# Performance work log

Measured on AMD Instinct MI355X. Metric: run time of the kernel, lower is better.

The kernel has to match this reference:

```python
import jax, jax.numpy as jnp
import numpy as np


def setup_inputs() -> dict:
    key = jax.random.key(0)
    kx, ka, kw = jax.random.split(key, 3)
    B, H, N, F = 8, 4, 1024, 128
    NHID = 128
    x = jax.random.normal(kx, (B, H, N, F), dtype=jnp.float32)
    adj = jax.random.uniform(ka, (B, H, N, N), dtype=jnp.float32)
    W = jax.random.normal(kw, (F, NHID), dtype=jnp.float32) / np.float32(np.sqrt(F))
    b = jnp.zeros((NHID,), dtype=jnp.float32)
    return {"x": x, "adj": adj, "W": W, "b": b}


def reference(x, adj, W, b):
    # x: [B, H, N, F], adj: [B, H, N, N]
    B, H, N, F = x.shape
    G = B * H
    k = (N * N) // int(N ** 0.5)  # top-k entries kept per (b,h) matrix

    # --- sparse_adj: keep global top-k entries of each N*N matrix ---
    flat = adj.reshape(G, N * N)
    vals, idx = jax.lax.top_k(flat, k)                    # [G, k]
    sparse = jnp.zeros_like(flat).at[jnp.arange(G)[:, None], idx].set(vals)
    sparse = sparse.reshape(G, N, N)

    # --- norm: symmetrize, then D^{-1/2} A D^{-1/2} ---
    s = (sparse + jnp.swapaxes(sparse, 1, 2)) * 0.5
    deg = jnp.sum(s, axis=-1)                             # [G, N]
    dinv = jnp.where(deg > 0, deg ** -0.5, 0.0)           # inf -> 0 as in torch
    norm_adj = dinv[:, :, None] * s * dinv[:, None, :]    # [G, N, N]

    # --- GIN conv with edge weights (eps = 0): ((1+eps)x + A_norm x) W + b ---
    # edge-list message passing over nonzeros of norm_adj == dense matmul
    xf = x.reshape(G, N, F)
    agg = jnp.einsum('gij,gjf->gif', norm_adj, xf)
    h = jax.nn.gelu((xf + agg) @ W + b, approximate=False)

    out = h.reshape(B, H, N, -1)                          # dropout: eval mode (identity)
    adj_copy = norm_adj                                   # [(B H), N, N]
    return out, adj_copy
```

## Files before the change

### kernel.cpp

```cpp
#include <hip/hip_runtime.h>
#include <math.h>

#define GG 32
#define NN1 1024
#define FF 128
#define MAT (NN1*NN1)
#define KKEEP 32768
#define NBINS 4096
#define CAP 8192
#define LCAP 1024
#define TIECAP 64
#define BINLO 1311
#define BINHI 1760

typedef __attribute__((ext_vector_type(8))) short short8;
typedef __attribute__((ext_vector_type(4))) float floatx4;
typedef __attribute__((ext_vector_type(8))) unsigned short ushort8;

__device__ __forceinline__ int fbin(float v) {
    int b = (int)((v - 0.95f) * 81920.0f);
    b = b < 0 ? 0 : (b > NBINS - 1 ? NBINS - 1 : b);
    return b;
}
__device__ __forceinline__ unsigned short f2bf(float f) {
    union { float f; unsigned u; } x; x.f = f;
    unsigned r = x.u + 0x7fffu + ((x.u >> 16) & 1u);
    return (unsigned short)(r >> 16);
}
__device__ __forceinline__ float bf2f(unsigned short h) {
    union { unsigned u; float f; } x; x.u = ((unsigned)h) << 16;
    return x.f;
}
__device__ __forceinline__ float gelu(float v) {
    return 0.5f * v * (1.0f + erff(v * 0.70710678118654752f));
}

__global__ __launch_bounds__(256) void k_histgather(const float* __restrict__ adj,
                                                    unsigned* __restrict__ hist,
                                                    uint2* __restrict__ cand,
                                                    unsigned* __restrict__ candCount) {
    __shared__ unsigned lh[NBINS];
    __shared__ uint2 lcand[LCAP];
    __shared__ unsigned lcnt;
    __shared__ unsigned gbase;
    int g = blockIdx.x >> 4, seg = blockIdx.x & 15;
    for (int i = threadIdx.x; i < NBINS; i += 256) lh[i] = 0;
    if (threadIdx.x == 0) lcnt = 0;
    __syncthreads();
    const float4* p = (const float4*)(adj + (size_t)g * MAT + (size_t)seg * 65536);
    for (int i = threadIdx.x; i < 16384; i += 256) {
        float4 v = p[i];
        unsigned base = (unsigned)(seg * 65536 + i * 4);
        float vv[4] = {v.x, v.y, v.z, v.w};
#pragma unroll
        for (int d = 0; d < 4; ++d) {
            if (vv[d] >= 0.95f) {
                int b = fbin(vv[d]);
                atomicAdd(&lh[b], 1u);
                if (b >= BINLO && b <= BINHI) {
                    unsigned pos = atomicAdd(&lcnt, 1u);
                    if (pos < LCAP) {
                        lcand[pos].x = __float_as_uint(vv[d]);
                        lcand[pos].y = base + (unsigned)d;
                    }
                }
            }
        }
    }
    __syncthreads();
    unsigned* gh = hist + g * NBINS;
    for (int i = threadIdx.x; i < NBINS; i += 256)
        if (lh[i]) atomicAdd(&gh[i], lh[i]);
    unsigned n = lcnt; if (n > LCAP) n = LCAP;
    if (threadIdx.x == 0) gbase = atomicAdd(&candCount[g], n);
    __syncthreads();
    unsigned gb = gbase;
    uint2* cg = cand + (size_t)g * CAP;
    for (unsigned i = threadIdx.x; i < n; i += 256) {
        unsigned pos = gb + i;
        if (pos < CAP) cg[pos] = lcand[i];
    }
}

__global__ __launch_bounds__(256) void k_selbin(const unsigned* __restrict__ hist,
                                                unsigned* __restrict__ binSel,
                                                unsigned* __restrict__ needArr) {
    int g = blockIdx.x;
    __shared__ unsigned csum[256];
    __shared__ unsigned after[256];
    const unsigned* gh = hist + g * NBINS;
    int t = threadIdx.x;
    unsigned s = 0;
    for (int i = 0; i < 16; ++i) s += gh[t * 16 + i];
    csum[t] = s;
    __syncthreads();
    if (t == 0) {
        unsigned run = 0;
        for (int c = 255; c >= 0; --c) { after[c] = run; run += csum[c]; }
    }
    __syncthreads();
    if (after[t] < (unsigned)KKEEP && after[t] + csum[t] >= (unsigned)KKEEP) {
        unsigned cum = after[t];
        for (int b2 = t * 16 + 15; b2 >= t * 16; --b2) {
            unsigned h = gh[b2];
            cum += h;
            if (cum >= (unsigned)KKEEP) {
                binSel[g] = (unsigned)b2;
                needArr[g] = (unsigned)KKEEP - (cum - h);
                break;
            }
        }
    }
}

__global__ __launch_bounds__(256) void k_rank(const uint2* __restrict__ cand,
                                              const unsigned* __restrict__ candCount,
                                              const unsigned* __restrict__ binSel,
                                              const unsigned* __restrict__ needArr,
                                              float* __restrict__ thr,
                                              unsigned* __restrict__ tieIdx,
                                              unsigned* __restrict__ tieCount) {
    int g = blockIdx.x;
    __shared__ uint2 mem[256];
    __shared__ unsigned mb;
    __shared__ float sT;
    unsigned m = candCount[g]; if (m > CAP) m = CAP;
    unsigned bsel = binSel[g];
    unsigned need = needArr[g];
    const uint2* cg = cand + (size_t)g * CAP;
    int t = threadIdx.x;
    if (t == 0) mb = 0;
    __syncthreads();
    for (unsigned ci = t; ci < m; ci += 256) {
        float v = __uint_as_float(cg[ci].x);
        if ((unsigned)fbin(v) == bsel) {
            unsigned i = atomicAdd(&mb, 1u);
            if (i < 256) mem[i] = cg[ci];
        }
    }
    __syncthreads();
    unsigned M = mb; if (M > 256) M = 256;
    unsigned rk = 0; float v = 0.f; unsigned idx = 0;
    if (t < (int)M) {
        v = __uint_as_float(mem[t].x);
        idx = mem[t].y;
        for (unsigned j = 0; j < M; ++j) {
            float vj = __uint_as_float(mem[j].x);
            if (vj > v || (vj == v && mem[j].y < idx)) ++rk;
        }
        if (rk == need - 1) sT = v;
    }
    __syncthreads();
    float T = sT;
    if (t == 0) thr[g] = T;
    if (t < (int)M && v == T && rk < need) {
        unsigned pos = atomicAdd(&tieCount[g], 1u);
        if (pos < TIECAP) tieIdx[g * TIECAP + pos] = idx;
    }
}

__device__ __forceinline__ float keepf(float v, unsigned idx, float T,
                                       const unsigned* __restrict__ tie, unsigned tc) {
    if (v > T) return v;
    if (v == T) {
        for (unsigned i = 0; i < tc; ++i)
            if (tie[i] == idx) return v;
    }
    return 0.f;
}

__global__ __launch_bounds__(256) void k_sym(const float* __restrict__ adj,
                                             const float* __restrict__ thr,
                                             const unsigned* __restrict__ tieIdx,
                                             const unsigned* __restrict__ tieCount,
                                             float* __restrict__ sOut,
                                             float* __restrict__ deg) {
    __shared__ float Al[64 * 65];
    __shared__ float Bl[64 * 65];
    int g = blockIdx.x / 136;
    int pr = blockIdx.x % 136;
    int ti = 0, rem = pr;
    while (rem >= 16 - ti) { rem -= 16 - ti; ++ti; }
    int tj = ti + rem;
    int t = threadIdx.x;
    float T = thr[g];
    unsigned tc = tieCount[g];
    if (tc > TIECAP) tc = TIECAP;
    const unsigned* tie = tieIdx + g * TIECAP;
    const float* ag = adj + (size_t)g * MAT;
    float* sg = sOut + (size_t)g * MAT;
    float* dg = deg + g * NN1;
    int r0 = t >> 4;
    int c0 = (t & 15) << 2;
    int i0 = ti << 6, j0 = tj << 6;
    bool off = (ti != tj);
    float av[4][4], bv[4][4];
#pragma unroll
    for (int q = 0; q < 4; ++q) {
        int r = r0 + (q << 4);
        unsigned base = (unsigned)((i0 + r) * NN1 + j0 + c0);
        float4 v = *(const float4*)(ag + base);
        av[q][0] = keepf(v.x, base + 0, T, tie, tc);
        av[q][1] = keepf(v.y, base + 1, T, tie, tc);
        av[q][2] = keepf(v.z, base + 2, T, tie, tc);
        av[q][3] = keepf(v.w, base + 3, T, tie, tc);
        Al[r * 65 + c0 + 0] = av[q][0];
        Al[r * 65 + c0 + 1] = av[q][1];
        Al[r * 65 + c0 + 2] = av[q][2];
        Al[r * 65 + c0 + 3] = av[q][3];
    }
    if (off) {
#pragma unroll
        for (int q = 0; q < 4; ++q) {
            int r = r0 + (q << 4);
            unsigned base = (unsigned)((j0 + r) * NN1 + i0 + c0);
            float4 v = *(const float4*)(ag + base);
            bv[q][0] = keepf(v.x, base + 0, T, tie, tc);
            bv[q][1] = keepf(v.y, base + 1, T, tie, tc);
            bv[q][2] = keepf(v.z, base + 2, T, tie, tc);
            bv[q][3] = keepf(v.w, base + 3, T, tie, tc);
            Bl[r * 65 + c0 + 0] = bv[q][0];
            Bl[r * 65 + c0 + 1] = bv[q][1];
            Bl[r * 65 + c0 + 2] = bv[q][2];
            Bl[r * 65 + c0 + 3] = bv[q][3];
        }
    }
    __syncthreads();
#pragma unroll
    for (int q = 0; q < 4; ++q) {
        int r = r0 + (q << 4);
        const float* Tr = off ? Bl : Al;
        float s0 = 0.5f * (av[q][0] + Tr[(c0 + 0) * 65 + r]);
        float s1 = 0.5f * (av[q][1] + Tr[(c0 + 1) * 65 + r]);
        float s2 = 0.5f * (av[q][2] + Tr[(c0 + 2) * 65 + r]);
        float s3 = 0.5f * (av[q][3] + Tr[(c0 + 3) * 65 + r]);
        *(float4*)(sg + (size_t)(i0 + r) * NN1 + j0 + c0) = make_float4(s0, s1, s2, s3);
        float rs = s0 + s1 + s2 + s3;
        rs += __shfl_xor(rs, 1);
        rs += __shfl_xor(rs, 2);
        rs += __shfl_xor(rs, 4);
        rs += __shfl_xor(rs, 8);
        if ((t & 15) == 0) atomicAdd(&dg[i0 + r], rs);
    }
    if (off) {
#pragma unroll
        for (int q = 0; q < 4; ++q) {
            int r = r0 + (q << 4);
            float s0 = 0.5f * (bv[q][0] + Al[(c0 + 0) * 65 + r]);
            float s1 = 0.5f * (bv[q][1] + Al[(c0 + 1) * 65 + r]);
            float s2 = 0.5f * (bv[q][2] + Al[(c0 + 2) * 65 + r]);
            float s3 = 0.5f * (bv[q][3] + Al[(c0 + 3) * 65 + r]);
            *(float4*)(sg + (size_t)(j0 + r) * NN1 + i0 + c0) = make_float4(s0, s1, s2, s3);
            float rs = s0 + s1 + s2 + s3;
            rs += __shfl_xor(rs, 1);
            rs += __shfl_xor(rs, 2);
            rs += __shfl_xor(rs, 4);
            rs += __shfl_xor(rs, 8);
            if ((t & 15) == 0) atomicAdd(&dg[j0 + r], rs);
        }
    }
}

__global__ __launch_bounds__(256) void k_dinv(const float* __restrict__ deg,
                                              float* __restrict__ dinv) {
    int i = blockIdx.x * 256 + threadIdx.x;
    float d = deg[i];
    dinv[i] = (d > 0.f) ? (float)(1.0 / sqrt((double)d)) : 0.f;
}

__global__ __launch_bounds__(256) void k_y(const float* __restrict__ x,
                                           const float* __restrict__ W,
                                           unsigned short* __restrict__ Yh,
                                           unsigned short* __restrict__ Yl) {
    __shared__ float Xl[64 * 128];
    int bx = blockIdx.x;
    int g = bx & 31, chunk = bx >> 5;
    int r0 = chunk * 64;
    int t = threadIdx.x;
    const float* xg = x + ((size_t)g * NN1 + r0) * FF;
    for (int i = t; i < 2048; i += 256) ((float4*)Xl)[i] = ((const float4*)xg)[i];
    __syncthreads();
    int Rr = (t >> 5) * 8;
    int c4 = (t & 31) * 4;
    float acc[8][4];
#pragma unroll
    for (int i = 0; i < 8; ++i)
#pragma unroll
        for (int j = 0; j < 4; ++j) acc[i][j] = 0.f;
    for (int f = 0; f < 128; ++f) {
        float4 wv = *(const float4*)(W + (size_t)f * 128 + c4);
#pragma unroll
        for (int i = 0; i < 8; ++i) {
            float a = Xl[(Rr + i) * 128 + f];
            acc[i][0] += a * wv.x;
            acc[i][1] += a * wv.y;
            acc[i][2] += a * wv.z;
            acc[i][3] += a * wv.w;
        }
    }
#pragma unroll
    for (int cc = 0; cc < 4; ++cc) {
        int c = c4 + cc;
        size_t base = ((size_t)g * 128 + c) * NN1 + r0 + Rr;
        ushort8 hh, ll;
#pragma unroll
        for (int i = 0; i < 8; ++i) {
            float v = acc[i][cc];
            unsigned short h = f2bf(v);
            hh[i] = h;
            ll[i] = f2bf(v - bf2f(h));
        }
        *(ushort8*)(Yh + base) = hh;
        *(ushort8*)(Yl + base) = ll;
    }
}

__global__ __launch_bounds__(256) void k_ng1(const unsigned short* __restrict__ Yh,
                                             const unsigned short* __restrict__ Yl,
                                             const float* __restrict__ dinv,
                                             float* __restrict__ sadj,
                                             const float* __restrict__ bias,
                                             float* __restrict__ hout) {
    __shared__ unsigned short AhL[32 * 40];
    __shared__ unsigned short AlL[32 * 40];
    int bx = blockIdx.x;
    int g = bx & 31, panel = bx >> 5;
    int r0 = panel * 32;
    int t = threadIdx.x;
    int w = t >> 6, lane = t & 63;
    int q = lane >> 4, n16 = lane & 15;
    float* sg = sadj + (size_t)g * MAT;
    const float* dv = dinv + g * NN1;
    int srow = t >> 3, skc = (t & 7) << 2;
    float drow = dv[r0 + srow];
    int cbase = w * 32;
    const unsigned short* yhg = Yh + (size_t)g * 128 * NN1;
    const unsigned short* ylg = Yl + (size_t)g * 128 * NN1;
    const unsigned short* ybh[2], *ybl[2];
#pragma unroll
    for (int ct = 0; ct < 2; ++ct) {
        size_t co = (size_t)(cbase + 16 * ct + n16) * NN1;
        ybh[ct] = yhg + co;
        ybl[ct] = ylg + co;
    }
    floatx4 acc[2][2];
#pragma unroll
    for (int i = 0; i < 2; ++i)
#pragma unroll
        for (int j = 0; j < 2; ++j) acc[i][j] = (floatx4){0.f, 0.f, 0.f, 0.f};

    for (int kt = 0; kt < 32; ++kt) {
        int k0 = kt << 5;
        float4 dj = *(const float4*)(dv + k0 + skc);
        float* ap = sg + (size_t)(r0 + srow) * NN1 + k0 + skc;
        float4 v = *(const float4*)ap;
        v.x *= drow * dj.x; v.y *= drow * dj.y;
        v.z *= drow * dj.z; v.w *= drow * dj.w;
        *(float4*)ap = v;
        float vv[4] = {v.x, v.y, v.z, v.w};
        ushort4 hh, ll;
        unsigned short* hp = (unsigned short*)&hh;
        unsigned short* lp = (unsigned short*)&ll;
#pragma unroll
        for (int d = 0; d < 4; ++d) {
            unsigned short h = f2bf(vv[d]);
            hp[d] = h;
            lp[d] = f2bf(vv[d] - bf2f(h));
        }
        *(ushort4*)(&AhL[srow * 40 + skc]) = hh;
        *(ushort4*)(&AlL[srow * 40 + skc]) = ll;
        __syncthreads();
        short8 ah[2], al[2], bh[2], bl[2];
#pragma unroll
        for (int rt = 0; rt < 2; ++rt) {
            ah[rt] = *(const short8*)(&AhL[(16 * rt + n16) * 40 + q * 8]);
            al[rt] = *(const short8*)(&AlL[(16 * rt + n16) * 40 + q * 8]);
        }
#pragma unroll
        for (int ct = 0; ct < 2; ++ct) {
            bh[ct] = *(const short8*)(ybh[ct] + k0 + q * 8);
            bl[ct] = *(const short8*)(ybl[ct] + k0 + q * 8);
        }
#pragma unroll
        for (int rt = 0; rt < 2; ++rt)
#pragma unroll
            for (int ct = 0; ct < 2; ++ct) {
                acc[rt][ct] = __builtin_amdgcn_mfma_f32_16x16x32_bf16(ah[rt], bh[ct], acc[rt][ct], 0, 0, 0);
                acc[rt][ct] = __builtin_amdgcn_mfma_f32_16x16x32_bf16(ah[rt], bl[ct], acc[rt][ct], 0, 0, 0);
                acc[rt][ct] = __builtin_amdgcn_mfma_f32_16x16x32_bf16(al[rt], bh[ct], acc[rt][ct], 0, 0, 0);
            }
        __syncthreads();
    }
    float* hg = hout + (size_t)g * NN1 * FF;
#pragma unroll
    for (int rt = 0; rt < 2; ++rt)
#pragma unroll
        for (int ct = 0; ct < 2; ++ct) {
            int c = cbase + 16 * ct + n16;
            float bb = bias[c];
#pragma unroll
            for (int reg = 0; reg < 4; ++reg) {
                int r = r0 + 16 * rt + 4 * q + reg;
                float yv = bf2f(ybh[ct][r]) + bf2f(ybl[ct][r]);
                float val = acc[rt][ct][reg] + yv + bb;
                hg[(size_t)r * FF + c] = gelu(val);
            }
        }
}

extern "C" void kernel_launch(void* const* d_in, const int* in_sizes, int n_in,
                              void* d_out, int out_size, void* d_ws, size_t ws_size,
                              hipStream_t stream) {
    const float* x = (const float*)d_in[0];
    const float* adj = (const float*)d_in[1];
    const float* W = (const float*)d_in[2];
    const float* b = (const float*)d_in[3];
    float* out = (float*)d_out;
    float* hout = out;
    float* adjn = out + (size_t)GG * NN1 * FF;

    char* ws = (char*)d_ws;
    unsigned* hist      = (unsigned*)(ws);
    unsigned* candCount = (unsigned*)(ws + 524288);
    unsigned* tieCount  = (unsigned*)(ws + 524416);
    float*    deg       = (float*)(ws + 524544);
    unsigned* binSel    = (unsigned*)(ws + 655616);
    unsigned* needArr   = (unsigned*)(ws + 655744);
    float*    thr       = (float*)(ws + 655872);
    unsigned* tieIdx    = (unsigned*)(ws + 656000);
    uint2*    cand      = (uint2*)(ws + 664192);
    float*    dinv      = (float*)(ws + 2761344);
    unsigned short* Yh  = (unsigned short*)(ws + 2892416);
    unsigned short* Yl  = (unsigned short*)(ws + 11281024);

    hipMemsetAsync(d_ws, 0, 655616, stream);

    k_histgather<<<512, 256, 0, stream>>>(adj, hist, cand, candCount);
    k_selbin<<<32, 256, 0, stream>>>(hist, binSel, needArr);
    k_rank<<<32, 256, 0, stream>>>(cand, candCount, binSel, needArr, thr, tieIdx, tieCount);
    k_sym<<<GG * 136, 256, 0, stream>>>(adj, thr, tieIdx, tieCount, adjn, deg);
    k_dinv<<<128, 256, 0, stream>>>(deg, dinv);
    k_y<<<512, 256, 0, stream>>>(x, W, Yh, Yl);
    k_ng1<<<1024, 256, 0, stream>>>(Yh, Yl, dinv, adjn, b, hout);
}
```

Measured before the change: 487.7 us.

## Double-buffer k_ng1 LDS tiles, prefetch adj rows, and use 64-row panels

The final normalize+aggregate kernel now processes 64-row panels instead of 32, so each block reuses the loaded Y column fragments across twice as many rows and the grid is halved. Adjacency loads for the next k-tile are issued one iteration ahead into registers. The LDS A tiles are double-buffered so one barrier per iteration suffices, and the dinv vector is staged in shared memory. The trade-off is more registers and LDS per block and fewer blocks to spread across the GPU.

New measurement: 473.1 us. -3.0%, faster.

```diff
diff --git a/kernel.cpp b/kernel.cpp
--- a/kernel.cpp
+++ b/kernel.cpp
@@ -321,17 +321,18 @@
                                              float* __restrict__ sadj,
                                              const float* __restrict__ bias,
                                              float* __restrict__ hout) {
-    __shared__ unsigned short AhL[32 * 40];
-    __shared__ unsigned short AlL[32 * 40];
+    __shared__ unsigned short AhL[2][64 * 40];
+    __shared__ unsigned short AlL[2][64 * 40];
+    __shared__ float DvL[NN1];
     int bx = blockIdx.x;
     int g = bx & 31, panel = bx >> 5;
-    int r0 = panel * 32;
+    int r0 = panel * 64;
     int t = threadIdx.x;
     int w = t >> 6, lane = t & 63;
     int q = lane >> 4, n16 = lane & 15;
     float* sg = sadj + (size_t)g * MAT;
     const float* dv = dinv + g * NN1;
-    int srow = t >> 3, skc = (t & 7) << 2;
+    int srow = t >> 2, skc = (t & 3) << 3;
     float drow = dv[r0 + srow];
     int cbase = w * 32;
     const unsigned short* yhg = Yh + (size_t)g * 128 * NN1;
@@ -343,57 +344,84 @@
         ybh[ct] = yhg + co;
         ybl[ct] = ylg + co;
     }
-    floatx4 acc[2][2];
-#pragma unroll
-    for (int i = 0; i < 2; ++i)
+    ((float4*)DvL)[t] = ((const float4*)dv)[t];
+
+    float* ap0 = sg + (size_t)(r0 + srow) * NN1 + skc;
+    float4 va = *(const float4*)ap0;
+    float4 vb = *(const float4*)(ap0 + 4);
+    __syncthreads();
+
+    floatx4 acc[4][2];
+#pragma unroll
+    for (int i = 0; i < 4; ++i)
 #pragma unroll
         for (int j = 0; j < 2; ++j) acc[i][j] = (floatx4){0.f, 0.f, 0.f, 0.f};
 
     for (int kt = 0; kt < 32; ++kt) {
         int k0 = kt << 5;
-        float4 dj = *(const float4*)(dv + k0 + skc);
-        float* ap = sg + (size_t)(r0 + srow) * NN1 + k0 + skc;
-        float4 v = *(const float4*)ap;
-        v.x *= drow * dj.x; v.y *= drow * dj.y;
-        v.z *= drow * dj.z; v.w *= drow * dj.w;
-        *(float4*)ap = v;
-        float vv[4] = {v.x, v.y, v.z, v.w};
-        ushort4 hh, ll;
-        unsigned short* hp = (unsigned short*)&hh;
-        unsigned short* lp = (unsigned short*)&ll;
+        int cur = kt & 1;
+        float4 cva = va, cvb = vb;
+        if (kt < 31) {
+            const float* apn = ap0 + k0 + 32;
+            va = *(const float4*)apn;
+            vb = *(const float4*)(apn + 4);
+        }
+        float4 dja = *(const float4*)&DvL[k0 + skc];
+        float4 djb = *(const float4*)&DvL[k0 + skc + 4];
+        cva.x *= drow * dja.x; cva.y *= drow * dja.y;
+        cva.z *= drow * dja.z; cva.w *= drow * dja.w;
+        cvb.x *= drow * djb.x; cvb.y *= drow * djb.y;
+        cvb.z *= drow * djb.z; cvb.w *= drow * djb.w;
+        float* ap = ap0 + k0;
+        *(float4*)ap = cva;
+        *(float4*)(ap + 4) = cvb;
+        float vv[8] = {cva.x, cva.y, cva.z, cva.w, cvb.x, cvb.y, cvb.z, cvb.w};
+        ushort4 hh0, ll0, hh1, ll1;
+        unsigned short* hp0 = (unsigned short*)&hh0;
+        unsigned short* lp0 = (unsigned short*)&ll0;
+        unsigned short* hp1 = (unsigned short*)&hh1;
+        unsigned short* lp1 = (unsigned short*)&ll1;
 #pragma unroll
         for (int d = 0; d < 4; ++d) {
             unsigned short h = f2bf(vv[d]);
-            hp[d] = h;
-            lp[d] = f2bf(vv[d] - bf2f(h));
-        }
-        *(ushort4*)(&AhL[srow * 40 + skc]) = hh;
-        *(ushort4*)(&AlL[srow * 40 + skc]) = ll;
-        __syncthreads();
-        short8 ah[2], al[2], bh[2], bl[2];
-#pragma unroll
-        for (int rt = 0; rt < 2; ++rt) {
-            ah[rt] = *(const short8*)(&AhL[(16 * rt + n16) * 40 + q * 8]);
-            al[rt] = *(const short8*)(&AlL[(16 * rt + n16) * 40 + q * 8]);
-        }
+            hp0[d] = h;
+            lp0[d] = f2bf(vv[d] - bf2f(h));
+        }
+#pragma unroll
+        for (int d = 0; d < 4; ++d) {
+            unsigned short h = f2bf(vv[4 + d]);
+            hp1[d] = h;
+            lp1[d] = f2bf(vv[4 + d] - bf2f(h));
+        }
+        *(ushort4*)(&AhL[cur][srow * 40 + skc]) = hh0;
+        *(ushort4*)(&AhL[cur][srow * 40 + skc + 4]) = hh1;
+        *(ushort4*)(&AlL[cur][srow * 40 + skc]) = ll0;
+        *(ushort4*)(&AlL[cur][srow * 40 + skc + 4]) = ll1;
+        short8 bh[2], bl[2];
 #pragma unroll
         for (int ct = 0; ct < 2; ++ct) {
             bh[ct] = *(const short8*)(ybh[ct] + k0 + q * 8);
             bl[ct] = *(const short8*)(ybl[ct] + k0 + q * 8);
         }
-#pragma unroll
-        for (int rt = 0; rt < 2; ++rt)
+        __syncthreads();
+        short8 ah[4], al[4];
+#pragma unroll
+        for (int rt = 0; rt < 4; ++rt) {
+            ah[rt] = *(const short8*)(&AhL[cur][(16 * rt + n16) * 40 + q * 8]);
+            al[rt] = *(const short8*)(&AlL[cur][(16 * rt + n16) * 40 + q * 8]);
+        }
+#pragma unroll
+        for (int rt = 0; rt < 4; ++rt)
 #pragma unroll
             for (int ct = 0; ct < 2; ++ct) {
                 acc[rt][ct] = __builtin_amdgcn_mfma_f32_16x16x32_bf16(ah[rt], bh[ct], acc[rt][ct], 0, 0, 0);
                 acc[rt][ct] = __builtin_amdgcn_mfma_f32_16x16x32_bf16(ah[rt], bl[ct], acc[rt][ct], 0, 0, 0);
                 acc[rt][ct] = __builtin_amdgcn_mfma_f32_16x16x32_bf16(al[rt], bh[ct], acc[rt][ct], 0, 0, 0);
             }
-        __syncthreads();
     }
     float* hg = hout + (size_t)g * NN1 * FF;
 #pragma unroll
-    for (int rt = 0; rt < 2; ++rt)
+    for (int rt = 0; rt < 4; ++rt)
 #pragma unroll
         for (int ct = 0; ct < 2; ++ct) {
             int c = cbase + 16 * ct + n16;
@@ -441,5 +469,5 @@
     k_sym<<<GG * 136, 256, 0, stream>>>(adj, thr, tieIdx, tieCount, adjn, deg);
     k_dinv<<<128, 256, 0, stream>>>(deg, dinv);
     k_y<<<512, 256, 0, stream>>>(x, W, Yh, Yl);
-    k_ng1<<<1024, 256, 0, stream>>>(Yh, Yl, dinv, adjn, b, hout);
-}
+    k_ng1<<<512, 256, 0, stream>>>(Yh, Yl, dinv, adjn, b, hout);
+}
```

## Double-buffer LDS tiles and prefetch adjacency two steps ahead in k_ng1

Applied to the files above, without the earlier changes.

The normalize-and-aggregate kernel now double-buffers its shared-memory A tiles, prefetches the adjacency float4s two k-steps ahead in registers, caches dinv in LDS, and unrolls the k loop by two. Only one barrier per step remains, so global loads can overlap the MFMA work and the second sync disappears. The macro is defined twice, and the first (buggy, al1*bl1) version is undefined before use, so only the correct one runs. The cost is extra LDS and registers, and the explicit waitcnt/sched_barrier sequencing may limit how the compiler schedules instructions.

Result: no change. 491.6 us (+0.8%).

```diff
diff --git a/kernel.cpp b/kernel.cpp
--- a/kernel.cpp
+++ b/kernel.cpp
@@ -321,8 +321,9 @@
                                              float* __restrict__ sadj,
                                              const float* __restrict__ bias,
                                              float* __restrict__ hout) {
-    __shared__ unsigned short AhL[32 * 40];
-    __shared__ unsigned short AlL[32 * 40];
+    __shared__ unsigned short AhL[2][32 * 40];
+    __shared__ unsigned short AlL[2][32 * 40];
+    __shared__ float DvL[NN1];
     int bx = blockIdx.x;
     int g = bx & 31, panel = bx >> 5;
     int r0 = panel * 32;
@@ -336,61 +337,132 @@
     int cbase = w * 32;
     const unsigned short* yhg = Yh + (size_t)g * 128 * NN1;
     const unsigned short* ylg = Yl + (size_t)g * 128 * NN1;
-    const unsigned short* ybh[2], *ybl[2];
-#pragma unroll
-    for (int ct = 0; ct < 2; ++ct) {
-        size_t co = (size_t)(cbase + 16 * ct + n16) * NN1;
-        ybh[ct] = yhg + co;
-        ybl[ct] = ylg + co;
-    }
+    const unsigned short* ybh0 = yhg + (size_t)(cbase + n16) * NN1;
+    const unsigned short* ybl0 = ylg + (size_t)(cbase + n16) * NN1;
+    const unsigned short* ybh1 = yhg + (size_t)(cbase + 16 + n16) * NN1;
+    const unsigned short* ybl1 = ylg + (size_t)(cbase + 16 + n16) * NN1;
+    ((float4*)DvL)[t] = ((const float4*)dv)[t];
+
+    float* ap0 = sg + (size_t)(r0 + srow) * NN1 + skc;
+    float4 pf0 = *(const float4*)ap0;
+    float4 pf1 = *(const float4*)(ap0 + 32);
+    __syncthreads();
+
     floatx4 acc[2][2];
 #pragma unroll
     for (int i = 0; i < 2; ++i)
 #pragma unroll
         for (int j = 0; j < 2; ++j) acc[i][j] = (floatx4){0.f, 0.f, 0.f, 0.f};
 
-    for (int kt = 0; kt < 32; ++kt) {
-        int k0 = kt << 5;
-        float4 dj = *(const float4*)(dv + k0 + skc);
-        float* ap = sg + (size_t)(r0 + srow) * NN1 + k0 + skc;
-        float4 v = *(const float4*)ap;
-        v.x *= drow * dj.x; v.y *= drow * dj.y;
-        v.z *= drow * dj.z; v.w *= drow * dj.w;
-        *(float4*)ap = v;
-        float vv[4] = {v.x, v.y, v.z, v.w};
-        ushort4 hh, ll;
-        unsigned short* hp = (unsigned short*)&hh;
-        unsigned short* lp = (unsigned short*)&ll;
-#pragma unroll
-        for (int d = 0; d < 4; ++d) {
-            unsigned short h = f2bf(vv[d]);
-            hp[d] = h;
-            lp[d] = f2bf(vv[d] - bf2f(h));
-        }
-        *(ushort4*)(&AhL[srow * 40 + skc]) = hh;
-        *(ushort4*)(&AlL[srow * 40 + skc]) = ll;
-        __syncthreads();
-        short8 ah[2], al[2], bh[2], bl[2];
-#pragma unroll
-        for (int rt = 0; rt < 2; ++rt) {
-            ah[rt] = *(const short8*)(&AhL[(16 * rt + n16) * 40 + q * 8]);
-            al[rt] = *(const short8*)(&AlL[(16 * rt + n16) * 40 + q * 8]);
-        }
-#pragma unroll
-        for (int ct = 0; ct < 2; ++ct) {
-            bh[ct] = *(const short8*)(ybh[ct] + k0 + q * 8);
-            bl[ct] = *(const short8*)(ybl[ct] + k0 + q * 8);
-        }
-#pragma unroll
-        for (int rt = 0; rt < 2; ++rt)
-#pragma unroll
-            for (int ct = 0; ct < 2; ++ct) {
-                acc[rt][ct] = __builtin_amdgcn_mfma_f32_16x16x32_bf16(ah[rt], bh[ct], acc[rt][ct], 0, 0, 0);
-                acc[rt][ct] = __builtin_amdgcn_mfma_f32_16x16x32_bf16(ah[rt], bl[ct], acc[rt][ct], 0, 0, 0);
-                acc[rt][ct] = __builtin_amdgcn_mfma_f32_16x16x32_bf16(al[rt], bh[ct], acc[rt][ct], 0, 0, 0);
-            }
-        __syncthreads();
-    }
+    int q8 = q * 8;
+
+#define NG_STEP(KT, PF)                                                          \
+    {                                                                            \
+        int k0 = (KT) << 5;                                                      \
+        int cur = (KT) & 1;                                                      \
+                       \
+        short8 bh0 = *(const short8*)(ybh0 + k0 + q8);                           \
+        short8 bl0 = *(const short8*)(ybl0 + k0 + q8);                           \
+        short8 bh1 = *(const short8*)(ybh1 + k0 + q8);                           \
+        short8 bl1 = *(const short8*)(ybl1 + k0 + q8);                           \
+                    \
+        float4 cva = (PF);                                                       \
+        int kn = (KT) + 2 < 32 ? (KT) + 2 : 31;                                  \
+        (PF) = *(const float4*)(ap0 + (kn << 5));                                \
+               \
+        float4 dja = *(const float4*)&DvL[k0 + skc];                             \
+        cva.x *= drow * dja.x; cva.y *= drow * dja.y;                            \
+        cva.z *= drow * dja.z; cva.w *= drow * dja.w;                            \
+        *(float4*)(ap0 + k0) = cva;                                              \
+        float vv0[4] = {cva.x, cva.y, cva.z, cva.w};                             \
+        ushort4 hh0, ll0;                                                        \
+        unsigned short* hp0 = (unsigned short*)&hh0;                             \
+        unsigned short* lp0 = (unsigned short*)&ll0;                             \
+        _Pragma("unroll")                                                        \
+        for (int d = 0; d < 4; ++d) {                                            \
+            unsigned short h = f2bf(vv0[d]);                                     \
+            hp0[d] = h;                                                          \
+            lp0[d] = f2bf(vv0[d] - bf2f(h));                                     \
+        }                                                                        \
+        *(ushort4*)(&AhL[cur][srow * 40 + skc]) = hh0;                           \
+        *(ushort4*)(&AlL[cur][srow * 40 + skc]) = ll0;                           \
+                     \
+        asm volatile("s_waitcnt lgkmcnt(0)" ::: "memory");                       \
+        __builtin_amdgcn_s_barrier();                                            \
+        __builtin_amdgcn_sched_barrier(0);                                       \
+        short8 ah0 = *(const short8*)(&AhL[cur][(n16) * 40 + q8]);               \
+        short8 al0 = *(const short8*)(&AlL[cur][(n16) * 40 + q8]);               \
+        short8 ah1 = *(const short8*)(&AhL[cur][(16 + n16) * 40 + q8]);          \
+        short8 al1 = *(const short8*)(&AlL[cur][(16 + n16) * 40 + q8]);          \
+        acc[0][0] = __builtin_amdgcn_mfma_f32_16x16x32_bf16(ah0, bh0, acc[0][0], 0, 0, 0); \
+        acc[0][0] = __builtin_amdgcn_mfma_f32_16x16x32_bf16(ah0, bl0, acc[0][0], 0, 0, 0); \
+        acc[0][0] = __builtin_amdgcn_mfma_f32_16x16x32_bf16(al0, bh0, acc[0][0], 0, 0, 0); \
+        acc[0][1] = __builtin_amdgcn_mfma_f32_16x16x32_bf16(ah0, bh1, acc[0][1], 0, 0, 0); \
+        acc[0][1] = __builtin_amdgcn_mfma_f32_16x16x32_bf16(ah0, bl1, acc[0][1], 0, 0, 0); \
+        acc[0][1] = __builtin_amdgcn_mfma_f32_16x16x32_bf16(al0, bh1, acc[0][1], 0, 0, 0); \
+        acc[1][0] = __builtin_amdgcn_mfma_f32_16x16x32_bf16(ah1, bh0, acc[1][0], 0, 0, 0); \
+        acc[1][0] = __builtin_amdgcn_mfma_f32_16x16x32_bf16(ah1, bl0, acc[1][0], 0, 0, 0); \
+        acc[1][0] = __builtin_amdgcn_mfma_f32_16x16x32_bf16(al1, bh0, acc[1][0], 0, 0, 0); \
+        acc[1][1] = __builtin_amdgcn_mfma_f32_16x16x32_bf16(ah1, bh1, acc[1][1], 0, 0, 0); \
+        acc[1][1] = __builtin_amdgcn_mfma_f32_16x16x32_bf16(ah1, bl1, acc[1][1], 0, 0, 0); \
+        acc[1][1] = __builtin_amdgcn_mfma_f32_16x16x32_bf16(al1, bl1 , acc[1][1], 0, 0, 0); \
+    }
+
+#undef NG_STEP
+#define NG_STEP(KT, PF)                                                          \
+    {                                                                            \
+        int k0 = (KT) << 5;                                                      \
+        int cur = (KT) & 1;                                                      \
+        short8 bh0 = *(const short8*)(ybh0 + k0 + q8);                           \
+        short8 bl0 = *(const short8*)(ybl0 + k0 + q8);                           \
+        short8 bh1 = *(const short8*)(ybh1 + k0 + q8);                           \
+        short8 bl1 = *(const short8*)(ybl1 + k0 + q8);                           \
+        float4 cva = (PF);                                                       \
+        int kn = (KT) + 2 < 32 ? (KT) + 2 : 31;                                  \
+        (PF) = *(const float4*)(ap0 + (kn << 5));                                \
+        float4 dja = *(const float4*)&DvL[k0 + skc];                             \
+        cva.x *= drow * dja.x; cva.y *= drow * dja.y;                            \
+        cva.z *= drow * dja.z; cva.w *= drow * dja.w;                            \
+        *(float4*)(ap0 + k0) = cva;                                              \
+        float vv0[4] = {cva.x, cva.y, cva.z, cva.w};                             \
+        ushort4 hh0, ll0;                                                        \
+        unsigned short* hp0 = (unsigned short*)&hh0;                             \
+        unsigned short* lp0 = (unsigned short*)&ll0;                             \
+        _Pragma("unroll")                                                        \
+        for (int d = 0; d < 4; ++d) {                                            \
+            unsigned short h = f2bf(vv0[d]);                                     \
+            hp0[d] = h;                                                          \
+            lp0[d] = f2bf(vv0[d] - bf2f(h));                                     \
+        }                                                                        \
+        *(ushort4*)(&AhL[cur][srow * 40 + skc]) = hh0;                           \
+        *(ushort4*)(&AlL[cur][srow * 40 + skc]) = ll0;                           \
+        asm volatile("s_waitcnt lgkmcnt(0)" ::: "memory");                       \
+        __builtin_amdgcn_s_barrier();                                            \
+        __builtin_amdgcn_sched_barrier(0);                                       \
+        short8 ah0 = *(const short8*)(&AhL[cur][(n16) * 40 + q8]);               \
+        short8 al0 = *(const short8*)(&AlL[cur][(n16) * 40 + q8]);               \
+        short8 ah1 = *(const short8*)(&AhL[cur][(16 + n16) * 40 + q8]);          \
+        short8 al1 = *(const short8*)(&AlL[cur][(16 + n16) * 40 + q8]);          \
+        acc[0][0] = __builtin_amdgcn_mfma_f32_16x16x32_bf16(ah0, bh0, acc[0][0], 0, 0, 0); \
+        acc[0][0] = __builtin_amdgcn_mfma_f32_16x16x32_bf16(ah0, bl0, acc[0][0], 0, 0, 0); \
+        acc[0][0] = __builtin_amdgcn_mfma_f32_16x16x32_bf16(al0, bh0, acc[0][0], 0, 0, 0); \
+        acc[0][1] = __builtin_amdgcn_mfma_f32_16x16x32_bf16(ah0, bh1, acc[0][1], 0, 0, 0); \
+        acc[0][1] = __builtin_amdgcn_mfma_f32_16x16x32_bf16(ah0, bl1, acc[0][1], 0, 0, 0); \
+        acc[0][1] = __builtin_amdgcn_mfma_f32_16x16x32_bf16(al0, bh1, acc[0][1], 0, 0, 0); \
+        acc[1][0] = __builtin_amdgcn_mfma_f32_16x16x32_bf16(ah1, bh0, acc[1][0], 0, 0, 0); \
+        acc[1][0] = __builtin_amdgcn_mfma_f32_16x16x32_bf16(ah1, bl0, acc[1][0], 0, 0, 0); \
+        acc[1][0] = __builtin_amdgcn_mfma_f32_16x16x32_bf16(al1, bh0, acc[1][0], 0, 0, 0); \
+        acc[1][1] = __builtin_amdgcn_mfma_f32_16x16x32_bf16(ah1, bh1, acc[1][1], 0, 0, 0); \
+        acc[1][1] = __builtin_amdgcn_mfma_f32_16x16x32_bf16(ah1, bl1, acc[1][1], 0, 0, 0); \
+        acc[1][1] = __builtin_amdgcn_mfma_f32_16x16x32_bf16(al1, bh1, acc[1][1], 0, 0, 0); \
+    }
+
+    for (int kt2 = 0; kt2 < 32; kt2 += 2) {
+        NG_STEP(kt2, pf0)
+        NG_STEP(kt2 + 1, pf1)
+    }
+#undef NG_STEP
+
     float* hg = hout + (size_t)g * NN1 * FF;
 #pragma unroll
     for (int rt = 0; rt < 2; ++rt)
@@ -398,10 +470,12 @@
         for (int ct = 0; ct < 2; ++ct) {
             int c = cbase + 16 * ct + n16;
             float bb = bias[c];
+            const unsigned short* yh_c = ct ? ybh1 : ybh0;
+            const unsigned short* yl_c = ct ? ybl1 : ybl0;
 #pragma unroll
             for (int reg = 0; reg < 4; ++reg) {
                 int r = r0 + 16 * rt + 4 * q + reg;
-                float yv = bf2f(ybh[ct][r]) + bf2f(ybl[ct][r]);
+                float yv = bf2f(yh_c[r]) + bf2f(yl_c[r]);
                 float val = acc[rt][ct][reg] + yv + bb;
                 hg[(size_t)r * FF + c] = gelu(val);
             }
```

## Load adjacency fragments directly into MFMA registers with two-step prefetch in k_ng1

Applied to the files above, without the earlier changes.

The k_ng1 kernel no longer stages the normalized adjacency tile through LDS. Each wave now loads its own A-fragment rows straight from global memory into registers, scales and splits them in registers, and prefetches the tile two k-steps ahead so loads overlap the MFMAs. Only one wave per row writes the normalized values back, and dinv is cached in LDS. This removes the LDS round-trip and one of the two barriers per iteration, but every wave loads the same A rows redundantly and register pressure rises.

Result: slower. 535.1 us (+9.7%).

```diff
diff --git a/kernel.cpp b/kernel.cpp
--- a/kernel.cpp
+++ b/kernel.cpp
@@ -315,82 +315,121 @@
     }
 }
 
+__device__ __forceinline__ void cvt8(const float4& a, const float4& b,
+                                     short8& hi, short8& lo) {
+    float v[8] = {a.x, a.y, a.z, a.w, b.x, b.y, b.z, b.w};
+#pragma unroll
+    for (int d = 0; d < 8; ++d) {
+        unsigned short h = f2bf(v[d]);
+        ((unsigned short*)&hi)[d] = h;
+        ((unsigned short*)&lo)[d] = f2bf(v[d] - bf2f(h));
+    }
+}
+
 __global__ __launch_bounds__(256) void k_ng1(const unsigned short* __restrict__ Yh,
                                              const unsigned short* __restrict__ Yl,
                                              const float* __restrict__ dinv,
                                              float* __restrict__ sadj,
                                              const float* __restrict__ bias,
                                              float* __restrict__ hout) {
-    __shared__ unsigned short AhL[32 * 40];
-    __shared__ unsigned short AlL[32 * 40];
+    __shared__ float DvL[NN1];
     int bx = blockIdx.x;
     int g = bx & 31, panel = bx >> 5;
     int r0 = panel * 32;
     int t = threadIdx.x;
     int w = t >> 6, lane = t & 63;
-    int q = lane >> 4, n16 = lane & 15;
+    int q = lane >> 4, n16 = lane & 15, q8 = q * 8;
     float* sg = sadj + (size_t)g * MAT;
     const float* dv = dinv + g * NN1;
-    int srow = t >> 3, skc = (t & 7) << 2;
-    float drow = dv[r0 + srow];
     int cbase = w * 32;
     const unsigned short* yhg = Yh + (size_t)g * 128 * NN1;
     const unsigned short* ylg = Yl + (size_t)g * 128 * NN1;
-    const unsigned short* ybh[2], *ybl[2];
-#pragma unroll
-    for (int ct = 0; ct < 2; ++ct) {
-        size_t co = (size_t)(cbase + 16 * ct + n16) * NN1;
-        ybh[ct] = yhg + co;
-        ybl[ct] = ylg + co;
-    }
+    const unsigned short* ybh0 = yhg + (size_t)(cbase + n16) * NN1;
+    const unsigned short* ybl0 = ylg + (size_t)(cbase + n16) * NN1;
+    const unsigned short* ybh1 = yhg + (size_t)(cbase + 16 + n16) * NN1;
+    const unsigned short* ybl1 = ylg + (size_t)(cbase + 16 + n16) * NN1;
+
+    int rowA = r0 + n16, rowB = r0 + 16 + n16;
+    float drA = dv[rowA], drB = dv[rowB];
+    float* apA = sg + (size_t)rowA * NN1 + q8;
+    float* apB = sg + (size_t)rowB * NN1 + q8;
+    bool wrA = (w < 2) && ((n16 >> 3) == w);
+    bool wrB = (w >= 2) && ((n16 >> 3) == w - 2);
+
+    ((float4*)DvL)[t] = ((const float4*)dv)[t];
+
+    float4 pA0a = *(const float4*)(apA);
+    float4 pA0b = *(const float4*)(apA + 4);
+    float4 pB0a = *(const float4*)(apB);
+    float4 pB0b = *(const float4*)(apB + 4);
+    float4 pA1a = *(const float4*)(apA + 32);
+    float4 pA1b = *(const float4*)(apA + 36);
+    float4 pB1a = *(const float4*)(apB + 32);
+    float4 pB1b = *(const float4*)(apB + 36);
+    __syncthreads();
+
     floatx4 acc[2][2];
 #pragma unroll
     for (int i = 0; i < 2; ++i)
 #pragma unroll
         for (int j = 0; j < 2; ++j) acc[i][j] = (floatx4){0.f, 0.f, 0.f, 0.f};
 
-    for (int kt = 0; kt < 32; ++kt) {
-        int k0 = kt << 5;
-        float4 dj = *(const float4*)(dv + k0 + skc);
-        float* ap = sg + (size_t)(r0 + srow) * NN1 + k0 + skc;
-        float4 v = *(const float4*)ap;
-        v.x *= drow * dj.x; v.y *= drow * dj.y;
-        v.z *= drow * dj.z; v.w *= drow * dj.w;
-        *(float4*)ap = v;
-        float vv[4] = {v.x, v.y, v.z, v.w};
-        ushort4 hh, ll;
-        unsigned short* hp = (unsigned short*)&hh;
-        unsigned short* lp = (unsigned short*)&ll;
-#pragma unroll
-        for (int d = 0; d < 4; ++d) {
-            unsigned short h = f2bf(vv[d]);
-            hp[d] = h;
-            lp[d] = f2bf(vv[d] - bf2f(h));
-        }
-        *(ushort4*)(&AhL[srow * 40 + skc]) = hh;
-        *(ushort4*)(&AlL[srow * 40 + skc]) = ll;
-        __syncthreads();
-        short8 ah[2], al[2], bh[2], bl[2];
-#pragma unroll
-        for (int rt = 0; rt < 2; ++rt) {
-            ah[rt] = *(const short8*)(&AhL[(16 * rt + n16) * 40 + q * 8]);
-            al[rt] = *(const short8*)(&AlL[(16 * rt + n16) * 40 + q * 8]);
-        }
-#pragma unroll
-        for (int ct = 0; ct < 2; ++ct) {
-            bh[ct] = *(const short8*)(ybh[ct] + k0 + q * 8);
-            bl[ct] = *(const short8*)(ybl[ct] + k0 + q * 8);
-        }
-#pragma unroll
-        for (int rt = 0; rt < 2; ++rt)
-#pragma unroll
-            for (int ct = 0; ct < 2; ++ct) {
-                acc[rt][ct] = __builtin_amdgcn_mfma_f32_16x16x32_bf16(ah[rt], bh[ct], acc[rt][ct], 0, 0, 0);
-                acc[rt][ct] = __builtin_amdgcn_mfma_f32_16x16x32_bf16(ah[rt], bl[ct], acc[rt][ct], 0, 0, 0);
-                acc[rt][ct] = __builtin_amdgcn_mfma_f32_16x16x32_bf16(al[rt], bh[ct], acc[rt][ct], 0, 0, 0);
-            }
-        __syncthreads();
-    }
+#define NG_STEP(KT, PA0, PA1, PB0, PB1)                                          \
+    {                                                                            \
+        int k0 = (KT) << 5;                                                      \
+              \
+        short8 bh0 = *(const short8*)(ybh0 + k0 + q8);                           \
+        short8 bl0 = *(const short8*)(ybl0 + k0 + q8);                           \
+        short8 bh1 = *(const short8*)(ybh1 + k0 + q8);                           \
+        short8 bl1 = *(const short8*)(ybl1 + k0 + q8);                           \
+                                                                   \
+        float4 dj0 = *(const float4*)&DvL[k0 + q8];                              \
+        float4 dj1 = *(const float4*)&DvL[k0 + q8 + 4];                          \
+                                           \
+        float4 sA0 = PA0, sA1 = PA1, sB0 = PB0, sB1 = PB1;                       \
+        sA0.x *= drA * dj0.x; sA0.y *= drA * dj0.y;                              \
+        sA0.z *= drA * dj0.z; sA0.w *= drA * dj0.w;                              \
+        sA1.x *= drA * dj1.x; sA1.y *= drA * dj1.y;                              \
+        sA1.z *= drA * dj1.z; sA1.w *= drA * dj1.w;                              \
+        sB0.x *= drB * dj0.x; sB0.y *= drB * dj0.y;                              \
+        sB0.z *= drB * dj0.z; sB0.w *= drB * dj0.w;                              \
+        sB1.x *= drB * dj1.x; sB1.y *= drB * dj1.y;                              \
+        sB1.z *= drB * dj1.z; sB1.w *= drB * dj1.w;                              \
+                                              \
+        short8 fAh, fAl, fBh, fBl;                                               \
+        cvt8(sA0, sA1, fAh, fAl);                                                \
+        cvt8(sB0, sB1, fBh, fBl);                                                \
+                \
+        asm volatile("" : "+v"(fAh), "+v"(fAl), "+v"(fBh), "+v"(fBl));           \
+        __builtin_amdgcn_s_barrier();                                            \
+        __builtin_amdgcn_sched_barrier(0);                                       \
+                         \
+        if (wrA) { *(float4*)(apA + k0) = sA0; *(float4*)(apA + k0 + 4) = sA1; } \
+        if (wrB) { *(float4*)(apB + k0) = sB0; *(float4*)(apB + k0 + 4) = sB1; } \
+            \
+        int kn = (KT) + 2 < 32 ? (KT) + 2 : 31; int ko = kn << 5;                \
+        PA0 = *(const float4*)(apA + ko); PA1 = *(const float4*)(apA + ko + 4);  \
+        PB0 = *(const float4*)(apB + ko); PB1 = *(const float4*)(apB + ko + 4);  \
+        acc[0][0] = __builtin_amdgcn_mfma_f32_16x16x32_bf16(fAh, bh0, acc[0][0], 0, 0, 0); \
+        acc[0][0] = __builtin_amdgcn_mfma_f32_16x16x32_bf16(fAh, bl0, acc[0][0], 0, 0, 0); \
+        acc[0][0] = __builtin_amdgcn_mfma_f32_16x16x32_bf16(fAl, bh0, acc[0][0], 0, 0, 0); \
+        acc[0][1] = __builtin_amdgcn_mfma_f32_16x16x32_bf16(fAh, bh1, acc[0][1], 0, 0, 0); \
+        acc[0][1] = __builtin_amdgcn_mfma_f32_16x16x32_bf16(fAh, bl1, acc[0][1], 0, 0, 0); \
+        acc[0][1] = __builtin_amdgcn_mfma_f32_16x16x32_bf16(fAl, bh1, acc[0][1], 0, 0, 0); \
+        acc[1][0] = __builtin_amdgcn_mfma_f32_16x16x32_bf16(fBh, bh0, acc[1][0], 0, 0, 0); \
+        acc[1][0] = __builtin_amdgcn_mfma_f32_16x16x32_bf16(fBh, bl0, acc[1][0], 0, 0, 0); \
+        acc[1][0] = __builtin_amdgcn_mfma_f32_16x16x32_bf16(fBl, bh0, acc[1][0], 0, 0, 0); \
+        acc[1][1] = __builtin_amdgcn_mfma_f32_16x16x32_bf16(fBh, bh1, acc[1][1], 0, 0, 0); \
+        acc[1][1] = __builtin_amdgcn_mfma_f32_16x16x32_bf16(fBh, bl1, acc[1][1], 0, 0, 0); \
+        acc[1][1] = __builtin_amdgcn_mfma_f32_16x16x32_bf16(fBl, bh1, acc[1][1], 0, 0, 0); \
+    }
+
+    for (int kt2 = 0; kt2 < 32; kt2 += 2) {
+        NG_STEP(kt2, pA0a, pA0b, pB0a, pB0b)
+        NG_STEP(kt2 + 1, pA1a, pA1b, pB1a, pB1b)
+    }
+#undef NG_STEP
+
     float* hg = hout + (size_t)g * NN1 * FF;
 #pragma unroll
     for (int rt = 0; rt < 2; ++rt)
@@ -398,10 +437,12 @@
         for (int ct = 0; ct < 2; ++ct) {
             int c = cbase + 16 * ct + n16;
             float bb = bias[c];
+            const unsigned short* yh_c = ct ? ybh1 : ybh0;
+            const unsigned short* yl_c = ct ? ybl1 : ybl0;
 #pragma unroll
             for (int reg = 0; reg < 4; ++reg) {
                 int r = r0 + 16 * rt + 4 * q + reg;
-                float yv = bf2f(ybh[ct][r]) + bf2f(ybl[ct][r]);
+                float yv = bf2f(yh_c[r]) + bf2f(yl_c[r]);
                 float val = acc[rt][ct][reg] + yv + bb;
                 hg[(size_t)r * FF + c] = gelu(val);
             }
```
